# Kernel optimization log

Measured on AMD Instinct MI355X. Metric: run time of the kernel, lower is better.

Reference implementation:

```python
import jax, jax.numpy as jnp
import numpy as np


def pfaffian(A):
    """Pfaffian of even-dim skew-symmetric A via Parlett-Reid LTL^T (no pivoting).
    pf(A) = prod over elimination steps of the (k, k+1) pivot."""
    n = A.shape[0]
    ar = jnp.arange(n)

    def step(carry, i):
        A, pf = carry
        k = 2 * i
        pivot = A[k, k + 1]
        mask = ar > (k + 1)                      # rows/cols k+2:
        tau = jnp.where(mask, A[k, :], 0.0) / pivot
        col = jnp.where(mask, A[:, k + 1], 0.0)
        # rank-2 skew update of the trailing submatrix
        A = A + tau[:, None] * col[None, :] - col[:, None] * tau[None, :]
        return (A, pf * pivot), None

    (A, pf), _ = jax.lax.scan(step, (A, jnp.ones((), A.dtype)), jnp.arange(n // 2))
    return pf


def setup_inputs() -> dict:
    key = jax.random.key(0)
    k1, k2 = jax.random.split(key)
    N = 128          # nsites; Nparticle = N (spin system, one particle per site)
    B = 128          # batch of Monte-Carlo configurations
    x = jax.random.normal(k1, (B, N), jnp.float32)
    scale = np.float32(np.sqrt(np.e / N))
    F = jax.random.normal(k2, (N * (2 * N - 1),), jnp.float32) * scale
    return {"x": x, "F": F}


def reference(x, F):
    N = x.shape[-1]
    Nparticle = N
    twoN = 2 * N
    # scatter parameter vector into strict lower triangle, antisymmetrize
    F_full = jnp.zeros((twoN, twoN), F.dtype).at[jnp.tril_indices(twoN, -1)].set(F)
    F_full = F_full - F_full.T

    def single(xi):
        # spin system: up orbitals where x>0, down orbitals where x<=0
        occ = jnp.concatenate([xi > 0, xi <= 0])
        idx = jnp.flatnonzero(occ, size=Nparticle)
        A = F_full[idx[:, None], idx[None, :]]   # [Nparticle, Nparticle] gather
        return pfaffian(A)

    return jax.vmap(single)(x)
```

## Files before the change

### kernel.cpp

```cpp
#include <hip/hip_runtime.h>


#define POFF(i) ((i) + (((i) >> 5) << 2))
#define RL(v, l) __int_as_float(__builtin_amdgcn_readlane(__float_as_int(v), (l)))

__global__ __launch_bounds__(512) void pfaffian_kernel(
    const float* __restrict__ x,
    const float* __restrict__ F,
    float* __restrict__ out)
{
    const int b    = blockIdx.x;
    const int t    = threadIdx.x;
    const int lane = t & 63;
    const int wave = t >> 6;

    __shared__ int idx_sh[128];
    __shared__ int wtot[4];
    __shared__ __align__(16) float tauLDS[2][4][144];
    __shared__ __align__(16) float colLDS[2][4][144];
    __shared__ __align__(16) float rS[2][4][144];
    __shared__ __align__(16) float cS[2][4][144];

    if (t < 256) {
        const float xv  = x[b * 128 + (t & 127)];
        const bool  pos = xv > 0.0f;
        const bool  o   = (t < 128) ? pos : !pos;
        const unsigned long long mm = __ballot(o);
        const int rank = __popcll(mm & ((1ull << lane) - 1ull));
        if (lane == 63) wtot[wave] = rank + (o ? 1 : 0);
        __syncthreads();
        int off = 0;
#pragma unroll
        for (int w = 0; w < 4; ++w)
            if (w < wave) off += wtot[w];
        if (o) idx_sh[off + rank] = t;
    } else {
        __syncthreads();
    }
    __syncthreads();

    if (wave == 0) __builtin_amdgcn_s_setprio(3);

    const int rg   = t >> 4;
    const int cg   = t & 15;
    const int row0 = rg << 2;
    const int col0 = cg << 3;
    const int prow = POFF(row0);
    const int pcol = POFF(col0);

    int ri[4], ci[8];
#pragma unroll
    for (int a = 0; a < 4; ++a) ri[a] = idx_sh[row0 + a];
#pragma unroll
    for (int c = 0; c < 8; ++c) ci[c] = idx_sh[col0 + c];

    float A[4][8];
#pragma unroll
    for (int a = 0; a < 4; ++a) {
        const int ii = ri[a];
#pragma unroll
        for (int c = 0; c < 8; ++c) {
            const int jj = ci[c];
            const int hi = ii > jj ? ii : jj;
            const int lo = ii > jj ? jj : ii;
            float v = (ii == jj) ? 0.0f : F[(hi * (hi - 1)) / 2 + lo];
            A[a][c] = (ii < jj) ? -v : v;
        }
    }

    auto stage = [&](int Pn, int st) {
        const int rgbase = 2 * Pn;
        if (rg == rgbase) {
            *(float4*)&rS[st][0][pcol]     = make_float4(A[0][0], A[0][1], A[0][2], A[0][3]);
            *(float4*)&rS[st][0][pcol + 4] = make_float4(A[0][4], A[0][5], A[0][6], A[0][7]);
            *(float4*)&rS[st][1][pcol]     = make_float4(A[2][0], A[2][1], A[2][2], A[2][3]);
            *(float4*)&rS[st][1][pcol + 4] = make_float4(A[2][4], A[2][5], A[2][6], A[2][7]);
        }
        if (rg == rgbase + 1) {
            *(float4*)&rS[st][2][pcol]     = make_float4(A[0][0], A[0][1], A[0][2], A[0][3]);
            *(float4*)&rS[st][2][pcol + 4] = make_float4(A[0][4], A[0][5], A[0][6], A[0][7]);
            *(float4*)&rS[st][3][pcol]     = make_float4(A[2][0], A[2][1], A[2][2], A[2][3]);
            *(float4*)&rS[st][3][pcol + 4] = make_float4(A[2][4], A[2][5], A[2][6], A[2][7]);
        }
        if (cg == Pn) {
            *(float4*)&cS[st][0][prow] = make_float4(A[0][1], A[1][1], A[2][1], A[3][1]);
            *(float4*)&cS[st][1][prow] = make_float4(A[0][3], A[1][3], A[2][3], A[3][3]);
            *(float4*)&cS[st][2][prow] = make_float4(A[0][5], A[1][5], A[2][5], A[3][5]);
            *(float4*)&cS[st][3][prow] = make_float4(A[0][7], A[1][7], A[2][7], A[3][7]);
        }
    };
    stage(0, 0);
    stage(1, 1);
    __syncthreads();

    float pf = 1.0f;

    auto crew = [&](int Pn, bool pre) {
        const int sv = Pn & 1;
        const int g0 = lane << 1;
        const int g1 = g0 + 1;
        const int pg = POFF(g0);
        float R[4][2], C[4][2];
#pragma unroll
        for (int j = 0; j < 4; ++j) {
            const float2 rv = *(const float2*)&rS[sv][j][pg];
            const float2 cv = *(const float2*)&cS[sv][j][pg];
            R[j][0] = rv.x; R[j][1] = rv.y;
            C[j][0] = cv.x; C[j][1] = cv.y;
        }
        if (pre) {
            const int svp  = sv ^ 1;
            const int base = POFF(8 * Pn);
            float4 Tq[4][2], Cq[4][2];
#pragma unroll
            for (int jp = 0; jp < 4; ++jp) {
                Tq[jp][0] = *(const float4*)&tauLDS[svp][jp][base];
                Tq[jp][1] = *(const float4*)&tauLDS[svp][jp][base + 4];
                Cq[jp][0] = *(const float4*)&colLDS[svp][jp][base];
                Cq[jp][1] = *(const float4*)&colLDS[svp][jp][base + 4];
            }
#pragma unroll
            for (int jp = 0; jp < 4; ++jp) {
                const float trA[4] = {Tq[jp][0].x, Tq[jp][0].z, Tq[jp][1].x, Tq[jp][1].z};
                const float crA[4] = {Cq[jp][0].x, Cq[jp][0].z, Cq[jp][1].x, Cq[jp][1].z};
                const float tcA[4] = {Tq[jp][0].y, Tq[jp][0].w, Tq[jp][1].y, Tq[jp][1].w};
                const float ccA[4] = {Cq[jp][0].y, Cq[jp][0].w, Cq[jp][1].y, Cq[jp][1].w};
                const float2 tpv = *(const float2*)&tauLDS[svp][jp][pg];
                const float2 cpv = *(const float2*)&colLDS[svp][jp][pg];
#pragma unroll
                for (int a = 0; a < 4; ++a) {
                    const float tau_r = trA[a];
                    const float col_r = crA[a];
                    R[a][0] = __fmaf_rn(-col_r, tpv.x,
                              __fmaf_rn(tau_r, cpv.x, R[a][0]));
                    R[a][1] = __fmaf_rn(-col_r, tpv.y,
                              __fmaf_rn(tau_r, cpv.y, R[a][1]));
                    const float tau_c = tcA[a];
                    const float col_c = ccA[a];
                    C[a][0] = __fmaf_rn(-cpv.x, tau_c,
                              __fmaf_rn(tpv.x, col_c, C[a][0]));
                    C[a][1] = __fmaf_rn(-cpv.y, tau_c,
                              __fmaf_rn(tpv.y, col_c, C[a][1]));
                }
            }
        }
        float TAU[4][2], CV[4][2];
#pragma unroll
        for (int j = 0; j < 4; ++j) {
            const int k = 8 * Pn + 2 * j;
            const float piv = RL(R[j][1], 4 * Pn + j);
            pf = __fmul_rn(pf, piv);
            TAU[j][0] = (g0 > k + 1) ? __fdiv_rn(R[j][0], piv) : 0.0f;
            TAU[j][1] = (g1 > k + 1) ? __fdiv_rn(R[j][1], piv) : 0.0f;
            CV[j][0]  = (g0 > k + 1) ? C[j][0] : 0.0f;
            CV[j][1]  = (g1 > k + 1) ? C[j][1] : 0.0f;
            *(float2*)&tauLDS[sv][j][pg] = make_float2(TAU[j][0], TAU[j][1]);
            *(float2*)&colLDS[sv][j][pg] = make_float2(CV[j][0], CV[j][1]);
#pragma unroll
            for (int j2 = j + 1; j2 < 4; ++j2) {
                const int ls = 4 * Pn + j2;
                const float tau_r = RL(TAU[j][0], ls);
                const float col_r = RL(CV[j][0], ls);
                R[j2][0] = __fmaf_rn(-col_r, TAU[j][0],
                           __fmaf_rn(tau_r, CV[j][0], R[j2][0]));
                R[j2][1] = __fmaf_rn(-col_r, TAU[j][1],
                           __fmaf_rn(tau_r, CV[j][1], R[j2][1]));
                const float tau_c = RL(TAU[j][1], ls);
                const float col_c = RL(CV[j][1], ls);
                C[j2][0] = __fmaf_rn(-CV[j][0], tau_c,
                           __fmaf_rn(TAU[j][0], col_c, C[j2][0]));
                C[j2][1] = __fmaf_rn(-CV[j][1], tau_c,
                           __fmaf_rn(TAU[j][1], col_c, C[j2][1]));
            }
        }
    };

    if (wave == 0) crew(0, false);
    __syncthreads();

    for (int P = 0; P < 15; ++P) {
        if (wave >= 1 && 2 * wave > P) {
            const int sp = P & 1;
#pragma unroll
            for (int j = 0; j < 4; ++j) {
                const float4 trv = *(const float4*)&tauLDS[sp][j][prow];
                const float4 crv = *(const float4*)&colLDS[sp][j][prow];
                const float4 t0v = *(const float4*)&tauLDS[sp][j][pcol];
                const float4 t1v = *(const float4*)&tauLDS[sp][j][pcol + 4];
                const float4 c0v = *(const float4*)&colLDS[sp][j][pcol];
                const float4 c1v = *(const float4*)&colLDS[sp][j][pcol + 4];
                const float tr[4] = {trv.x, trv.y, trv.z, trv.w};
                const float cr[4] = {crv.x, crv.y, crv.z, crv.w};
                const float tc[8] = {t0v.x, t0v.y, t0v.z, t0v.w,
                                     t1v.x, t1v.y, t1v.z, t1v.w};
                const float cc[8] = {c0v.x, c0v.y, c0v.z, c0v.w,
                                     c1v.x, c1v.y, c1v.z, c1v.w};
#pragma unroll
                for (int a = 0; a < 4; ++a) {
#pragma unroll
                    for (int c = 0; c < 8; ++c) {
                        A[a][c] = __fmaf_rn(-cr[a], tc[c],
                                  __fmaf_rn(tr[a], cc[c], A[a][c]));
                    }
                }
            }
            if (P <= 13) stage(P + 2, P & 1);
        }
        if (wave == 0) crew(P + 1, true);
        __syncthreads();
    }

    if (t == 0) out[b] = pf;
}

extern "C" void kernel_launch(void* const* d_in, const int* in_sizes, int n_in,
                              void* d_out, int out_size, void* d_ws, size_t ws_size,
                              hipStream_t stream) {
    const float* x = (const float*)d_in[0];
    const float* F = (const float*)d_in[1];
    float* out     = (float*)d_out;
    (void)in_sizes; (void)n_in; (void)out_size; (void)d_ws; (void)ws_size;

    pfaffian_kernel<<<128, 512, 0, stream>>>(x, F, out);
}
```

Before: 76.04 us.

## Double threads per block and shrink per-thread tile to 2x8 rows

```diff
diff --git a/kernel.cpp b/kernel.cpp
--- a/kernel.cpp
+++ b/kernel.cpp
@@ -4,7 +4,7 @@
 #define POFF(i) ((i) + (((i) >> 5) << 2))
 #define RL(v, l) __int_as_float(__builtin_amdgcn_readlane(__float_as_int(v), (l)))
 
-__global__ __launch_bounds__(512) void pfaffian_kernel(
+__global__ __launch_bounds__(1024) void pfaffian_kernel(
     const float* __restrict__ x,
     const float* __restrict__ F,
     float* __restrict__ out)
@@ -39,24 +39,22 @@
     }
     __syncthreads();
 
-    if (wave == 0) __builtin_amdgcn_s_setprio(3);
-
     const int rg   = t >> 4;
     const int cg   = t & 15;
-    const int row0 = rg << 2;
+    const int row0 = rg << 1;
     const int col0 = cg << 3;
     const int prow = POFF(row0);
     const int pcol = POFF(col0);
 
-    int ri[4], ci[8];
-#pragma unroll
-    for (int a = 0; a < 4; ++a) ri[a] = idx_sh[row0 + a];
+    int ri[2], ci[8];
+#pragma unroll
+    for (int a = 0; a < 2; ++a) ri[a] = idx_sh[row0 + a];
 #pragma unroll
     for (int c = 0; c < 8; ++c) ci[c] = idx_sh[col0 + c];
 
-    float A[4][8];
-#pragma unroll
-    for (int a = 0; a < 4; ++a) {
+    float A[2][8];
+#pragma unroll
+    for (int a = 0; a < 2; ++a) {
         const int ii = ri[a];
 #pragma unroll
         for (int c = 0; c < 8; ++c) {
@@ -69,24 +67,16 @@
     }
 
     auto stage = [&](int Pn, int st) {
-        const int rgbase = 2 * Pn;
-        if (rg == rgbase) {
-            *(float4*)&rS[st][0][pcol]     = make_float4(A[0][0], A[0][1], A[0][2], A[0][3]);
-            *(float4*)&rS[st][0][pcol + 4] = make_float4(A[0][4], A[0][5], A[0][6], A[0][7]);
-            *(float4*)&rS[st][1][pcol]     = make_float4(A[2][0], A[2][1], A[2][2], A[2][3]);
-            *(float4*)&rS[st][1][pcol + 4] = make_float4(A[2][4], A[2][5], A[2][6], A[2][7]);
-        }
-        if (rg == rgbase + 1) {
-            *(float4*)&rS[st][2][pcol]     = make_float4(A[0][0], A[0][1], A[0][2], A[0][3]);
-            *(float4*)&rS[st][2][pcol + 4] = make_float4(A[0][4], A[0][5], A[0][6], A[0][7]);
-            *(float4*)&rS[st][3][pcol]     = make_float4(A[2][0], A[2][1], A[2][2], A[2][3]);
-            *(float4*)&rS[st][3][pcol + 4] = make_float4(A[2][4], A[2][5], A[2][6], A[2][7]);
+        const int d = rg - 4 * Pn;
+        if (d >= 0 && d < 4) {
+            *(float4*)&rS[st][d][pcol]     = make_float4(A[0][0], A[0][1], A[0][2], A[0][3]);
+            *(float4*)&rS[st][d][pcol + 4] = make_float4(A[0][4], A[0][5], A[0][6], A[0][7]);
         }
         if (cg == Pn) {
-            *(float4*)&cS[st][0][prow] = make_float4(A[0][1], A[1][1], A[2][1], A[3][1]);
-            *(float4*)&cS[st][1][prow] = make_float4(A[0][3], A[1][3], A[2][3], A[3][3]);
-            *(float4*)&cS[st][2][prow] = make_float4(A[0][5], A[1][5], A[2][5], A[3][5]);
-            *(float4*)&cS[st][3][prow] = make_float4(A[0][7], A[1][7], A[2][7], A[3][7]);
+            *(float2*)&cS[st][0][prow] = make_float2(A[0][1], A[1][1]);
+            *(float2*)&cS[st][1][prow] = make_float2(A[0][3], A[1][3]);
+            *(float2*)&cS[st][2][prow] = make_float2(A[0][5], A[1][5]);
+            *(float2*)&cS[st][3][prow] = make_float2(A[0][7], A[1][7]);
         }
     };
     stage(0, 0);
@@ -179,24 +169,24 @@
     __syncthreads();
 
     for (int P = 0; P < 15; ++P) {
-        if (wave >= 1 && 2 * wave > P) {
+        if (wave > P) {
             const int sp = P & 1;
 #pragma unroll
             for (int j = 0; j < 4; ++j) {
-                const float4 trv = *(const float4*)&tauLDS[sp][j][prow];
-                const float4 crv = *(const float4*)&colLDS[sp][j][prow];
+                const float2 trv = *(const float2*)&tauLDS[sp][j][prow];
+                const float2 crv = *(const float2*)&colLDS[sp][j][prow];
                 const float4 t0v = *(const float4*)&tauLDS[sp][j][pcol];
                 const float4 t1v = *(const float4*)&tauLDS[sp][j][pcol + 4];
                 const float4 c0v = *(const float4*)&colLDS[sp][j][pcol];
                 const float4 c1v = *(const float4*)&colLDS[sp][j][pcol + 4];
-                const float tr[4] = {trv.x, trv.y, trv.z, trv.w};
-                const float cr[4] = {crv.x, crv.y, crv.z, crv.w};
+                const float tr[2] = {trv.x, trv.y};
+                const float cr[2] = {crv.x, crv.y};
                 const float tc[8] = {t0v.x, t0v.y, t0v.z, t0v.w,
                                      t1v.x, t1v.y, t1v.z, t1v.w};
                 const float cc[8] = {c0v.x, c0v.y, c0v.z, c0v.w,
                                      c1v.x, c1v.y, c1v.z, c1v.w};
 #pragma unroll
-                for (int a = 0; a < 4; ++a) {
+                for (int a = 0; a < 2; ++a) {
 #pragma unroll
                     for (int c = 0; c < 8; ++c) {
                         A[a][c] = __fmaf_rn(-cr[a], tc[c],
@@ -221,5 +211,5 @@
     float* out     = (float*)d_out;
     (void)in_sizes; (void)n_in; (void)out_size; (void)d_ws; (void)ws_size;
 
-    pfaffian_kernel<<<128, 512, 0, stream>>>(x, F, out);
+    pfaffian_kernel<<<128, 1024, 0, stream>>>(x, F, out);
 }
```

After: 78.74 us. +3.5%, slower.
